# Kernel tuning notes

Hardware: AMD Instinct MI355X
Metric: run time of the kernel (lower is better)

Reference implementation:

```python
import jax, jax.numpy as jnp
import numpy as np

N = 50000        # nodes
E = 800000       # edges (before self-loops)
F_IN = 256       # n_features
HID = 32         # hidden_dims (per-head out channels)
HEADS = 4
HC = HID * HEADS # 128, per-layer width
CLASSES = 40
LAYERS = 2
SLOPE = 0.1      # negative_slope for leaky_relu in attention


def _glorot(key, shape):
    fan_in, fan_out = shape[-2], shape[-1]
    lim = np.sqrt(6.0 / (fan_in + fan_out))
    return jax.random.uniform(key, shape, jnp.float32, -lim, lim)


def setup_inputs() -> dict:
    key = jax.random.key(0)
    ks = jax.random.split(key, 7)
    x = jax.random.normal(ks[0], (N, F_IN), jnp.float32)
    edge_index = jax.random.randint(ks[1], (2, E), 0, N, jnp.int64)
    weight_in = _glorot(ks[2], (F_IN, HC))
    weight_out = _glorot(ks[3], (HC, CLASSES))
    Ws = _glorot(ks[4], (LAYERS, HC, HC))            # per-layer GATConv linear
    atts = _glorot(ks[5], (LAYERS, HEADS, 2 * HID))  # [a_src | a_dst] per head
    biases = jnp.zeros((LAYERS, HC), jnp.float32)
    return {"x": x, "edge_index": edge_index, "weight_in": weight_in,
            "Ws": Ws, "atts": atts, "biases": biases, "weight_out": weight_out}


def _gat_conv(h, src, dst, W, att, bias):
    # h: [N, HC]; src/dst: [E'] edge endpoints (message src -> dst)
    n = h.shape[0]
    hp = (h @ W).reshape(n, HEADS, HID)                       # [N, H, C]
    a_src, a_dst = att[:, :HID], att[:, HID:]                 # [H, C] each
    alpha_src = jnp.einsum('nhc,hc->nh', hp, a_src)           # [N, H]
    alpha_dst = jnp.einsum('nhc,hc->nh', hp, a_dst)
    logits = jax.nn.leaky_relu(alpha_src[src] + alpha_dst[dst], SLOPE)  # [E', H]
    # softmax over edges grouped by destination node
    m = jax.ops.segment_max(logits, dst, num_segments=n)      # [N, H]
    e = jnp.exp(logits - m[dst])
    z = jax.ops.segment_sum(e, dst, num_segments=n)           # [N, H]
    alpha = e / z[dst]                                        # [E', H]
    msg = hp[src] * alpha[:, :, None]                         # [E', H, C]
    out = jax.ops.segment_sum(msg, dst, num_segments=n)       # [N, H, C]
    return out.reshape(n, HC) + bias


def reference(x, edge_index, weight_in, Ws, atts, biases, weight_out):
    # add self-loops (PyG GATConv default)
    loop = jnp.arange(N, dtype=edge_index.dtype)
    src = jnp.concatenate([edge_index[0], loop])
    dst = jnp.concatenate([edge_index[1], loop])
    h = x @ weight_in
    for l in range(LAYERS):
        # dropout is identity in eval mode
        h = jax.nn.elu(_gat_conv(h, src, dst, Ws[l], atts[l], biases[l]))
    return jax.nn.log_softmax(h @ weight_out, axis=1)
```

## Files before the change

kernel.cpp:

```cpp
#include <hip/hip_runtime.h>
#include <hip/hip_bf16.h>
#include <math.h>

#define N_NODES 50000
#define N_EDGES 800000
#define F_IN 256
#define HID 32
#define HEADS 4
#define HC 128
#define CLASSES 40
#define LAYERS 2
#define SLOPE 0.1f
#define EE (N_EDGES + N_NODES)

#define BSHIFT 9
#define NBUCK 98
#define CHUNK 4096
#define NBLK_E ((EE + CHUNK - 1) / CHUNK)
#define GEMM_BLOCKS ((N_NODES + 63) / 64)

typedef unsigned short ushortT;
typedef unsigned int uintT;
typedef __attribute__((ext_vector_type(8))) short short8v;
typedef __attribute__((ext_vector_type(4))) float f32x4;

__device__ __forceinline__ ushortT f2bu(float f) {
    __hip_bfloat16 h = __float2bfloat16(f);
    ushortT u; __builtin_memcpy(&u, &h, 2); return u;
}

__device__ __forceinline__ void scan_buckets(const int* __restrict__ bcnt,
                                             int* sbase, int t) {
    if (t < 64) {
        int i0 = 2 * t, i1 = 2 * t + 1;
        int v0 = (i0 < NBUCK) ? bcnt[i0] : 0;
        int v1 = (i1 < NBUCK) ? bcnt[i1] : 0;
        int s = v0 + v1;
        int x = s;
#pragma unroll
        for (int off = 1; off < 64; off <<= 1) {
            int y = __shfl_up(x, off);
            if (t >= off) x += y;
        }
        int excl = x - s;
        if (i0 <= NBUCK) sbase[i0] = excl;
        if (i1 <= NBUCK) sbase[i1] = excl + v0;
    }
    __syncthreads();
}

__global__ void wconv_all(const float* __restrict__ w_in, const float* __restrict__ Ws,
                          const float* __restrict__ w_out, ushortT* __restrict__ w_inT,
                          ushortT* __restrict__ WsT, ushortT* __restrict__ woutT,
                          int* __restrict__ bcnt, int* __restrict__ gcur0,
                          int* __restrict__ rowptr) {
    int i = blockIdx.x * 256 + threadIdx.x;
    if (i < NBUCK) { bcnt[i] = 0; gcur0[i] = 0; }
    if (i == NBUCK) rowptr[N_NODES] = EE;
    if (i < 32768) {
        int r = i >> 7, c = i & 127;
        w_inT[(size_t)c * F_IN + r] = f2bu(w_in[i]);
    } else if (i < 65536) {
        int j = i - 32768;
        int l = j >> 14, jj = j & 16383;
        int r = jj >> 7, c = jj & 127;
        WsT[l * 16384 + c * 128 + r] = f2bu(Ws[j]);
    } else if (i < 65536 + 6144) {
        int j = i - 65536;
        int c = j >> 7, k = j & 127;
        woutT[j] = (c < CLASSES) ? f2bu(w_out[k * CLASSES + c]) : (ushortT)0;
    }
}

#define AS_LD 40
template<bool AF32>
__device__ __forceinline__ void gemm_body(ushortT* As, ushortT* Bs,
                                          const void* __restrict__ Aptr,
                                          const ushortT* __restrict__ BT,
                                          ushortT* __restrict__ Cb,
                                          const float* __restrict__ att,
                                          float* __restrict__ asrc,
                                          float* __restrict__ adst,
                                          int M, int K, int bid) {
    int t = threadIdx.x;
    int w = t >> 6, lane = t & 63;
    int row0 = bid * 64;
    int ar = t >> 2, ak = (t & 3) * 8;
    int bcol = t >> 1, bks = (t & 1) * 16;
    int wr = w * 16;
    int arow = wr + (lane & 15);
    int ak8 = (lane >> 4) * 8;
    f32x4 acc[8] = {};

    for (int k0 = 0; k0 < K; k0 += 32) {
        int grow = row0 + ar;
        if (AF32) {
            const float* A = (const float*)Aptr;
            float4 v0 = make_float4(0.f, 0.f, 0.f, 0.f), v1 = v0;
            if (grow < M) {
                const float* ap = A + (size_t)grow * K + k0 + ak;
                v0 = *(const float4*)ap;
                v1 = *(const float4*)(ap + 4);
            }
            uint4 p;
            p.x = (uintT)f2bu(v0.x) | ((uintT)f2bu(v0.y) << 16);
            p.y = (uintT)f2bu(v0.z) | ((uintT)f2bu(v0.w) << 16);
            p.z = (uintT)f2bu(v1.x) | ((uintT)f2bu(v1.y) << 16);
            p.w = (uintT)f2bu(v1.z) | ((uintT)f2bu(v1.w) << 16);
            *(uint4*)&As[ar * AS_LD + ak] = p;
        } else {
            const ushortT* A = (const ushortT*)Aptr;
            uint4 p = make_uint4(0, 0, 0, 0);
            if (grow < M) p = *(const uint4*)(A + (size_t)grow * K + k0 + ak);
            *(uint4*)&As[ar * AS_LD + ak] = p;
        }
        {
            const ushortT* bp = BT + (size_t)bcol * K + k0 + bks;
            *(uint4*)&Bs[bcol * AS_LD + bks]     = *(const uint4*)bp;
            *(uint4*)&Bs[bcol * AS_LD + bks + 8] = *(const uint4*)(bp + 8);
        }
        __syncthreads();
        short8v a = *(short8v*)&As[arow * AS_LD + ak8];
#pragma unroll
        for (int c = 0; c < 8; ++c) {
            short8v b = *(short8v*)&Bs[(c * 16 + (lane & 15)) * AS_LD + ak8];
            acc[c] = __builtin_amdgcn_mfma_f32_16x16x32_bf16(a, b, acc[c], 0, 0, 0);
        }
        __syncthreads();
    }
    int cl = lane & 15;
    int r0 = row0 + wr + ((lane >> 4) << 2);
#pragma unroll
    for (int c = 0; c < 8; ++c) {
        int cc = c * 16 + cl;
#pragma unroll
        for (int r = 0; r < 4; ++r) {
            int rr = r0 + r;
            if (rr < M) Cb[(size_t)rr * 128 + cc] = f2bu(acc[c][r]);
        }
    }
    if (att) {
#pragma unroll
        for (int h = 0; h < HEADS; ++h) {
            float as0 = att[h * 64 + cl];
            float as1 = att[h * 64 + 16 + cl];
            float ad0 = att[h * 64 + 32 + cl];
            float ad1 = att[h * 64 + 48 + cl];
#pragma unroll
            for (int r = 0; r < 4; ++r) {
                float ps = acc[2 * h][r] * as0 + acc[2 * h + 1][r] * as1;
                float pd = acc[2 * h][r] * ad0 + acc[2 * h + 1][r] * ad1;
#pragma unroll
                for (int off = 1; off < 16; off <<= 1) {
                    ps += __shfl_xor(ps, off);
                    pd += __shfl_xor(pd, off);
                }
                int rr = r0 + r;
                if (cl == 0 && rr < M) {
                    asrc[rr * 4 + h] = ps;
                    adst[rr * 4 + h] = pd;
                }
            }
        }
    }
}

template<bool AF32>
__global__ __launch_bounds__(256) void gemm_mfma(const void* __restrict__ Aptr,
                                                 const ushortT* __restrict__ BT,
                                                 ushortT* __restrict__ Cb,
                                                 const float* __restrict__ att,
                                                 float* __restrict__ asrc,
                                                 float* __restrict__ adst,
                                                 int M, int K) {
    __shared__ ushortT As[64 * AS_LD];
    __shared__ ushortT Bs[128 * AS_LD];
    gemm_body<AF32>(As, Bs, Aptr, BT, Cb, att, asrc, adst, M, K, blockIdx.x);
}

__device__ __forceinline__ void csr_local_body(const uintT* __restrict__ ebuf,
                                               const int* __restrict__ bcnt,
                                               int* __restrict__ rowptr,
                                               int* __restrict__ ssrc, int b,
                                               int* sbase, int* cnt, int* cur,
                                               int* wsum) {
    int t = threadIdx.x;
    scan_buckets(bcnt, sbase, t);
    int node0 = b << BSHIFT;
    int nb = min(512, N_NODES - node0);
    int beg = sbase[b], end = sbase[b + 1];
    cnt[t] = 0; cnt[t + 256] = 0;
    __syncthreads();
    for (int i = beg + t; i < end; i += 256)
        atomicAdd(&cnt[ebuf[i] & 511], 1);
    __syncthreads();
    int v0 = cnt[2 * t], v1 = cnt[2 * t + 1];
    int s = v0 + v1;
    int lane = t & 63, w = t >> 6;
    int x = s;
#pragma unroll
    for (int off = 1; off < 64; off <<= 1) { int y = __shfl_up(x, off); if (lane >= off) x += y; }
    if (lane == 63) wsum[w] = x;
    __syncthreads();
    if (t == 0) { int run = 0; for (int k = 0; k < 4; ++k) { int tmp = wsum[k]; wsum[k] = run; run += tmp; } }
    __syncthreads();
    int excl = wsum[w] + x - s;
    cnt[2 * t] = excl; cnt[2 * t + 1] = excl + v0;
    cur[2 * t] = excl; cur[2 * t + 1] = excl + v0;
    if (2 * t < nb)     rowptr[node0 + 2 * t]     = beg + excl;
    if (2 * t + 1 < nb) rowptr[node0 + 2 * t + 1] = beg + excl + v0;
    __syncthreads();
    for (int i = beg + t; i < end; i += 256) {
        uintT e = ebuf[i];
        int pos = beg + atomicAdd(&cur[e & 511], 1);
        ssrc[pos] = (int)(e >> BSHIFT);
    }
}

__global__ __launch_bounds__(256) void gemm0_count(const float* __restrict__ x,
                                                   const ushortT* __restrict__ w_inT,
                                                   ushortT* __restrict__ hb0,
                                                   const int* __restrict__ ei,
                                                   int* __restrict__ bcnt) {
    __shared__ ushortT As[64 * AS_LD];
    __shared__ ushortT Bs[128 * AS_LD];
    __shared__ int hist[NBUCK];
    if (blockIdx.x < GEMM_BLOCKS) {
        gemm_body<true>(As, Bs, x, w_inT, hb0, nullptr, nullptr, nullptr,
                        N_NODES, F_IN, blockIdx.x);
    } else {
        int t = threadIdx.x;
        if (t < NBUCK) hist[t] = 0;
        __syncthreads();
        int base = (blockIdx.x - GEMM_BLOCKS) * CHUNK;
        int end = min(base + CHUNK, EE);
        for (int i = base + t; i < end; i += 256) {
            int d = (i < N_EDGES) ? ei[N_EDGES + i] : (i - N_EDGES);
            atomicAdd(&hist[d >> BSHIFT], 1);
        }
        __syncthreads();
        if (t < NBUCK && hist[t]) atomicAdd(&bcnt[t], hist[t]);
    }
}

__global__ __launch_bounds__(256) void gemm_csr(const ushortT* __restrict__ hin,
                                                const ushortT* __restrict__ BT,
                                                ushortT* __restrict__ hpb,
                                                const float* __restrict__ att,
                                                float* __restrict__ asrc,
                                                float* __restrict__ adst,
                                                const uintT* __restrict__ ebuf,
                                                const int* __restrict__ bcnt,
                                                int* __restrict__ rowptr,
                                                int* __restrict__ ssrc) {
    __shared__ ushortT As[64 * AS_LD];
    __shared__ ushortT Bs[128 * AS_LD];
    __shared__ int sbase[NBUCK + 2];
    __shared__ int cnt[512];
    __shared__ int cur[512];
    __shared__ int wsum[4];
    if (blockIdx.x < GEMM_BLOCKS) {
        gemm_body<false>(As, Bs, hin, BT, hpb, att, asrc, adst,
                         N_NODES, HC, blockIdx.x);
    } else {
        csr_local_body(ebuf, bcnt, rowptr, ssrc, blockIdx.x - GEMM_BLOCKS,
                       sbase, cnt, cur, wsum);
    }
}

__global__ __launch_bounds__(256) void bucket_scatter(const int* __restrict__ ei,
                                                      const int* __restrict__ bcnt,
                                                      int* __restrict__ gcur0,
                                                      uintT* __restrict__ ebuf) {
    __shared__ int sbase[NBUCK + 2];
    __shared__ int hist[NBUCK];
    __shared__ int rbase[NBUCK];
    int t = threadIdx.x;
    scan_buckets(bcnt, sbase, t);
    if (t < NBUCK) hist[t] = 0;
    __syncthreads();
    int base = blockIdx.x * CHUNK;
    int end = min(base + CHUNK, EE);
    for (int i = base + t; i < end; i += 256) {
        int d = (i < N_EDGES) ? ei[N_EDGES + i] : (i - N_EDGES);
        atomicAdd(&hist[d >> BSHIFT], 1);
    }
    __syncthreads();
    if (t < NBUCK) {
        int c = hist[t];
        rbase[t] = c ? (sbase[t] + atomicAdd(&gcur0[t], c)) : 0;
    }
    __syncthreads();
    if (t < NBUCK) hist[t] = 0;
    __syncthreads();
    for (int i = base + t; i < end; i += 256) {
        int s, d;
        if (i < N_EDGES) { s = ei[i]; d = ei[N_EDGES + i]; } else { s = d = i - N_EDGES; }
        int b = d >> BSHIFT;
        int pos = rbase[b] + atomicAdd(&hist[b], 1);
        ebuf[pos] = ((uintT)s << BSHIFT) | (uintT)(d & 511);
    }
}

__global__ __launch_bounds__(256) void cls_mfma(const ushortT* __restrict__ A,
                                                const ushortT* __restrict__ BT,
                                                float* __restrict__ out, int M) {
    __shared__ ushortT As[64 * AS_LD];
    __shared__ ushortT Bs[48 * AS_LD];
    int t = threadIdx.x;
    int w = t >> 6, lane = t & 63;
    int row0 = blockIdx.x * 64;
    int ar = t >> 2, ak = (t & 3) * 8;
    int wr = w * 16;
    int arow = wr + (lane & 15);
    int ak8 = (lane >> 4) * 8;
    f32x4 acc[3] = {};

    for (int k0 = 0; k0 < 128; k0 += 32) {
        int grow = row0 + ar;
        uint4 p = make_uint4(0, 0, 0, 0);
        if (grow < M) p = *(const uint4*)(A + (size_t)grow * 128 + k0 + ak);
        *(uint4*)&As[ar * AS_LD + ak] = p;
        if (t < 96) {
            int bcol = t >> 1, bks = (t & 1) * 16;
            const ushortT* bp = BT + bcol * 128 + k0 + bks;
            *(uint4*)&Bs[bcol * AS_LD + bks]     = *(const uint4*)bp;
            *(uint4*)&Bs[bcol * AS_LD + bks + 8] = *(const uint4*)(bp + 8);
        }
        __syncthreads();
        short8v a = *(short8v*)&As[arow * AS_LD + ak8];
#pragma unroll
        for (int c = 0; c < 3; ++c) {
            short8v b = *(short8v*)&Bs[(c * 16 + (lane & 15)) * AS_LD + ak8];
            acc[c] = __builtin_amdgcn_mfma_f32_16x16x32_bf16(a, b, acc[c], 0, 0, 0);
        }
        __syncthreads();
    }
    int cl = lane & 15;
    int r0 = row0 + wr + ((lane >> 4) << 2);
#pragma unroll
    for (int r = 0; r < 4; ++r) {
        float v0 = acc[0][r], v1 = acc[1][r];
        float v2 = (cl < 8) ? acc[2][r] : -1e30f;
        float m = fmaxf(fmaxf(v0, v1), v2);
#pragma unroll
        for (int off = 1; off < 16; off <<= 1) m = fmaxf(m, __shfl_xor(m, off));
        float e = __expf(v0 - m) + __expf(v1 - m) + ((cl < 8) ? __expf(v2 - m) : 0.f);
#pragma unroll
        for (int off = 1; off < 16; off <<= 1) e += __shfl_xor(e, off);
        float ls = m + __logf(e);
        int rr = r0 + r;
        if (rr < M) {
            float* o = out + (size_t)rr * CLASSES;
            o[cl] = v0 - ls;
            o[16 + cl] = v1 - ls;
            if (cl < 8) o[32 + cl] = v2 - ls;
        }
    }
}

__device__ __forceinline__ float lrelu(float v) { return v > 0.f ? v : SLOPE * v; }

__device__ __forceinline__ void gat_one(
    int node, int beg, int deg, int lane,
    const int* __restrict__ ssrc, const float* __restrict__ asrc,
    const float* __restrict__ adst, const ushortT* __restrict__ hpb,
    const float* __restrict__ bias, ushortT* __restrict__ foutB,
    float* sexp, int* ssrcl, float* sm)
{
    float4 ad = *(const float4*)(adst + (size_t)node * 4);
    int g = lane >> 4, i0 = lane & 15;
    float acc0 = 0.f, acc1 = 0.f;
    float zinv;
    const ushortT* hrow = hpb + lane * 2;

    if (deg <= 64) {
        float4 lg = make_float4(-1e30f, -1e30f, -1e30f, -1e30f);
        int soff = 0;
        if (lane < deg) {
            int s = ssrc[beg + lane];
            float4 a = *(const float4*)(asrc + (size_t)s * 4);
            lg.x = lrelu(a.x + ad.x);
            lg.y = lrelu(a.y + ad.y);
            lg.z = lrelu(a.z + ad.z);
            lg.w = lrelu(a.w + ad.w);
            soff = s * HC;
        }
        ssrcl[lane] = soff;
        *(float4*)&sexp[lane * 4] = lg;
        asm volatile("s_waitcnt lgkmcnt(0)" ::: "memory");
        float mg =     sexp[i0 * 4 + g];
        mg = fmaxf(mg, sexp[(i0 + 16) * 4 + g]);
        mg = fmaxf(mg, sexp[(i0 + 32) * 4 + g]);
        mg = fmaxf(mg, sexp[(i0 + 48) * 4 + g]);
#pragma unroll
        for (int off = 1; off < 16; off <<= 1) mg = fmaxf(mg, __shfl_xor(mg, off));
        if (i0 == 0) sm[g] = mg;
        asm volatile("s_waitcnt lgkmcnt(0)" ::: "memory");
        float4 m = *(float4*)&sm[0];
        float4 ex;
        ex.x = __expf(lg.x - m.x);
        ex.y = __expf(lg.y - m.y);
        ex.z = __expf(lg.z - m.z);
        ex.w = __expf(lg.w - m.w);
        *(float4*)&sexp[lane * 4] = ex;
        asm volatile("s_waitcnt lgkmcnt(0)" ::: "memory");
        float zg = sexp[i0 * 4 + g];
        zg +=      sexp[(i0 + 16) * 4 + g];
        zg +=      sexp[(i0 + 32) * 4 + g];
        zg +=      sexp[(i0 + 48) * 4 + g];
#pragma unroll
        for (int off = 1; off < 16; off <<= 1) zg += __shfl_xor(zg, off);
        zinv = 1.f / zg;
#pragma unroll 4
        for (int i = 0; i < deg; ++i) {
            float e = sexp[i * 4 + g];
            int off = ssrcl[i];
            uintT u = *(const uintT*)(hrow + off);
            acc0 = fmaf(__uint_as_float(u << 16),         e, acc0);
            acc1 = fmaf(__uint_as_float(u & 0xffff0000u), e, acc1);
        }
    } else {
        float4 m = make_float4(-1e30f, -1e30f, -1e30f, -1e30f);
        for (int i = lane; i < deg; i += 64) {
            int s = ssrc[beg + i];
            float4 a = *(const float4*)(asrc + (size_t)s * 4);
            m.x = fmaxf(m.x, lrelu(a.x + ad.x));
            m.y = fmaxf(m.y, lrelu(a.y + ad.y));
            m.z = fmaxf(m.z, lrelu(a.z + ad.z));
            m.w = fmaxf(m.w, lrelu(a.w + ad.w));
        }
#pragma unroll
        for (int off = 1; off < 64; off <<= 1) {
            m.x = fmaxf(m.x, __shfl_xor(m.x, off));
            m.y = fmaxf(m.y, __shfl_xor(m.y, off));
            m.z = fmaxf(m.z, __shfl_xor(m.z, off));
            m.w = fmaxf(m.w, __shfl_xor(m.w, off));
        }
        float4 zp = make_float4(0.f, 0.f, 0.f, 0.f);
        for (int c0 = 0; c0 < deg; c0 += 64) {
            int n_ch = min(64, deg - c0);
            if (lane < n_ch) {
                int s = ssrc[beg + c0 + lane];
                float4 a = *(const float4*)(asrc + (size_t)s * 4);
                float4 ex;
                ex.x = __expf(lrelu(a.x + ad.x) - m.x);
                ex.y = __expf(lrelu(a.y + ad.y) - m.y);
                ex.z = __expf(lrelu(a.z + ad.z) - m.z);
                ex.w = __expf(lrelu(a.w + ad.w) - m.w);
                *(float4*)&sexp[lane * 4] = ex;
                ssrcl[lane] = s * HC;
                zp.x += ex.x; zp.y += ex.y; zp.z += ex.z; zp.w += ex.w;
            }
            asm volatile("s_waitcnt lgkmcnt(0)" ::: "memory");
#pragma unroll 4
            for (int i = 0; i < n_ch; ++i) {
                float e = sexp[i * 4 + g];
                int off = ssrcl[i];
                uintT u = *(const uintT*)(hrow + off);
                acc0 = fmaf(__uint_as_float(u << 16),         e, acc0);
                acc1 = fmaf(__uint_as_float(u & 0xffff0000u), e, acc1);
            }
        }
#pragma unroll
        for (int off = 1; off < 64; off <<= 1) {
            zp.x += __shfl_xor(zp.x, off);
            zp.y += __shfl_xor(zp.y, off);
            zp.z += __shfl_xor(zp.z, off);
            zp.w += __shfl_xor(zp.w, off);
        }
        float zh = (g == 0) ? zp.x : (g == 1) ? zp.y : (g == 2) ? zp.z : zp.w;
        zinv = 1.f / zh;
    }

    float b0 = bias[lane * 2], b1 = bias[lane * 2 + 1];
    float v0 = acc0 * zinv + b0; v0 = v0 > 0.f ? v0 : __expf(v0) - 1.f;
    float v1 = acc1 * zinv + b1; v1 = v1 > 0.f ? v1 : __expf(v1) - 1.f;
    *(uintT*)(foutB + (size_t)node * HC + lane * 2) =
        (uintT)f2bu(v0) | ((uintT)f2bu(v1) << 16);
}

#define WPB 4
__global__ __launch_bounds__(256) void gat_gather2(
    const int* __restrict__ rowptr, const int* __restrict__ ssrc,
    const float* __restrict__ asrc, const float* __restrict__ adst,
    const ushortT* __restrict__ hpb, const float* __restrict__ bias,
    ushortT* __restrict__ foutB)
{
    __shared__ __align__(16) float s_exp[WPB][64][4];
    __shared__ int   s_src[WPB][64];
    __shared__ __align__(16) float s_m[WPB][8];
    __shared__ __align__(16) float s_z[WPB][8];
    int w = threadIdx.x >> 6;
    int lane = threadIdx.x & 63;
    int widx = blockIdx.x * WPB + w;
    int n0 = widx * 2;
    if (n0 >= N_NODES) return;
    int beg0 = rowptr[n0];
    int mid  = rowptr[n0 + 1];
    int end1 = rowptr[n0 + 2];
    int deg0 = mid - beg0, deg1 = end1 - mid;

    if (deg0 <= 32 && deg1 <= 32) {
        int half = lane >> 5;
        int ll = lane & 31;
        int nn = n0 + half;
        int mybeg = half ? mid : beg0;
        int mydeg = half ? deg1 : deg0;
        float4 ad = *(const float4*)(adst + (size_t)nn * 4);
        float4 lg = make_float4(-1e30f, -1e30f, -1e30f, -1e30f);
        int soff = 0;
        if (ll < mydeg) {
            int s = ssrc[mybeg + ll];
            float4 a = *(const float4*)(asrc + (size_t)s * 4);
            lg.x = lrelu(a.x + ad.x);
            lg.y = lrelu(a.y + ad.y);
            lg.z = lrelu(a.z + ad.z);
            lg.w = lrelu(a.w + ad.w);
            soff = s * HC;
        }
        s_src[w][lane] = soff;
        *(float4*)&s_exp[w][lane][0] = lg;
        asm volatile("s_waitcnt lgkmcnt(0)" ::: "memory");
        int grp = lane >> 3, gi = lane & 7;
        int gbase = (grp >> 2) << 5;
        int gh = grp & 3;
        float mg =     s_exp[w][gbase + gi][gh];
        mg = fmaxf(mg, s_exp[w][gbase + gi +  8][gh]);
        mg = fmaxf(mg, s_exp[w][gbase + gi + 16][gh]);
        mg = fmaxf(mg, s_exp[w][gbase + gi + 24][gh]);
        mg = fmaxf(mg, __shfl_xor(mg, 1));
        mg = fmaxf(mg, __shfl_xor(mg, 2));
        mg = fmaxf(mg, __shfl_xor(mg, 4));
        if (gi == 0) s_m[w][grp] = mg;
        asm volatile("s_waitcnt lgkmcnt(0)" ::: "memory");
        float4 m = *(float4*)&s_m[w][half * 4];
        float4 ex;
        ex.x = __expf(lg.x - m.x);
        ex.y = __expf(lg.y - m.y);
        ex.z = __expf(lg.z - m.z);
        ex.w = __expf(lg.w - m.w);
        *(float4*)&s_exp[w][lane][0] = ex;
        asm volatile("s_waitcnt lgkmcnt(0)" ::: "memory");
        float zg = s_exp[w][gbase + gi][gh];
        zg +=      s_exp[w][gbase + gi +  8][gh];
        zg +=      s_exp[w][gbase + gi + 16][gh];
        zg +=      s_exp[w][gbase + gi + 24][gh];
        zg += __shfl_xor(zg, 1);
        zg += __shfl_xor(zg, 2);
        zg += __shfl_xor(zg, 4);
        if (gi == 0) s_z[w][grp] = zg;
        asm volatile("s_waitcnt lgkmcnt(0)" ::: "memory");
        int hd = ll >> 3;
        float zinv = 1.f / s_z[w][half * 4 + hd];
        int maxdeg = max(deg0, deg1);
        int ebase = half << 5;
        const ushortT* hrow = hpb + ll * 4;
        float a0 = 0.f, a1 = 0.f, a2 = 0.f, a3 = 0.f;
#pragma unroll 4
        for (int i = 0; i < maxdeg; ++i) {
            float e = s_exp[w][ebase + i][hd];
            int off = s_src[w][ebase + i];
            uint2 u = *(const uint2*)(hrow + off);
            a0 = fmaf(__uint_as_float(u.x << 16),         e, a0);
            a1 = fmaf(__uint_as_float(u.x & 0xffff0000u), e, a1);
            a2 = fmaf(__uint_as_float(u.y << 16),         e, a2);
            a3 = fmaf(__uint_as_float(u.y & 0xffff0000u), e, a3);
        }
        const float* bp = bias + ll * 4;
        float v0 = a0 * zinv + bp[0]; v0 = v0 > 0.f ? v0 : __expf(v0) - 1.f;
        float v1 = a1 * zinv + bp[1]; v1 = v1 > 0.f ? v1 : __expf(v1) - 1.f;
        float v2 = a2 * zinv + bp[2]; v2 = v2 > 0.f ? v2 : __expf(v2) - 1.f;
        float v3 = a3 * zinv + bp[3]; v3 = v3 > 0.f ? v3 : __expf(v3) - 1.f;
        uint2 o;
        o.x = (uintT)f2bu(v0) | ((uintT)f2bu(v1) << 16);
        o.y = (uintT)f2bu(v2) | ((uintT)f2bu(v3) << 16);
        *(uint2*)(foutB + (size_t)nn * HC + ll * 4) = o;
    } else {
        gat_one(n0,     beg0, deg0, lane, ssrc, asrc, adst, hpb, bias, foutB,
                &s_exp[w][0][0], &s_src[w][0], &s_m[w][0]);
        gat_one(n0 + 1, mid,  deg1, lane, ssrc, asrc, adst, hpb, bias, foutB,
                &s_exp[w][0][0], &s_src[w][0], &s_m[w][0]);
    }
}

extern "C" void kernel_launch(void* const* d_in, const int* in_sizes, int n_in,
                              void* d_out, int out_size, void* d_ws, size_t ws_size,
                              hipStream_t stream) {
    const float* x      = (const float*)d_in[0];
    const int*   ei     = (const int*)d_in[1];
    const float* w_in   = (const float*)d_in[2];
    const float* Ws     = (const float*)d_in[3];
    const float* atts   = (const float*)d_in[4];
    const float* biases = (const float*)d_in[5];
    const float* w_out  = (const float*)d_in[6];
    float* out = (float*)d_out;

    char* wp = (char*)d_ws;
    ushortT* hb0 = (ushortT*)wp; wp += (size_t)N_NODES * HC * 2;
    ushortT* hb1 = (ushortT*)wp; wp += (size_t)N_NODES * HC * 2;
    ushortT* hpb = (ushortT*)wp; wp += (size_t)N_NODES * HC * 2;
    float* asrc  = (float*)wp;   wp += (size_t)N_NODES * HEADS * 4;
    float* adst  = (float*)wp;   wp += (size_t)N_NODES * HEADS * 4;
    int* rowptr  = (int*)wp;     wp += (size_t)(N_NODES + 4) * 4;
    int* ssrc    = (int*)wp;     wp += (size_t)EE * 4;
    uintT* ebuf  = (uintT*)wp;   wp += (size_t)EE * 4;
    int* bcnt    = (int*)wp;     wp += (size_t)(NBUCK + 4) * 4;
    int* gcur0   = (int*)wp;     wp += (size_t)(NBUCK + 4) * 4;
    ushortT* w_inT = (ushortT*)wp; wp += (size_t)HC * F_IN * 2;
    ushortT* WsT   = (ushortT*)wp; wp += (size_t)LAYERS * HC * HC * 2;
    ushortT* woutT = (ushortT*)wp; wp += (size_t)48 * HC * 2;

    wconv_all<<<(32768 + 32768 + 6144 + 255) / 256, 256, 0, stream>>>(
        w_in, Ws, w_out, w_inT, WsT, woutT, bcnt, gcur0, rowptr);

    gemm0_count<<<GEMM_BLOCKS + NBLK_E, 256, 0, stream>>>(x, w_inT, hb0, ei, bcnt);

    bucket_scatter<<<NBLK_E, 256, 0, stream>>>(ei, bcnt, gcur0, ebuf);

    gemm_csr<<<GEMM_BLOCKS + NBUCK, 256, 0, stream>>>(
        hb0, WsT, hpb, atts, asrc, adst, ebuf, bcnt, rowptr, ssrc);

    int g2blk = (N_NODES / 2 + WPB - 1) / WPB;
    gat_gather2<<<g2blk, 64 * WPB, 0, stream>>>(
        rowptr, ssrc, asrc, adst, hpb, biases, hb1);

    gemm_mfma<false><<<GEMM_BLOCKS, 256, 0, stream>>>(
        hb1, WsT + (size_t)HC * HC, hpb, atts + (size_t)HEADS * 2 * HID,
        asrc, adst, N_NODES, HC);
    gat_gather2<<<g2blk, 64 * WPB, 0, stream>>>(
        rowptr, ssrc, asrc, adst, hpb, biases + HC, hb0);

    cls_mfma<<<GEMM_BLOCKS, 256, 0, stream>>>(hb0, woutT, out, N_NODES);
}
```

Before: 165.9 us.

## Fuse edge bucketing into one pass using fixed-capacity buckets

```diff
diff --git a/kernel.cpp b/kernel.cpp
--- a/kernel.cpp
+++ b/kernel.cpp
@@ -15,6 +15,7 @@
 
 #define BSHIFT 9
 #define NBUCK 98
+#define BCAP 16384
 #define CHUNK 4096
 #define NBLK_E ((EE + CHUNK - 1) / CHUNK)
 #define GEMM_BLOCKS ((N_NODES + 63) / 64)
@@ -29,34 +30,12 @@
     ushortT u; __builtin_memcpy(&u, &h, 2); return u;
 }
 
-__device__ __forceinline__ void scan_buckets(const int* __restrict__ bcnt,
-                                             int* sbase, int t) {
-    if (t < 64) {
-        int i0 = 2 * t, i1 = 2 * t + 1;
-        int v0 = (i0 < NBUCK) ? bcnt[i0] : 0;
-        int v1 = (i1 < NBUCK) ? bcnt[i1] : 0;
-        int s = v0 + v1;
-        int x = s;
-#pragma unroll
-        for (int off = 1; off < 64; off <<= 1) {
-            int y = __shfl_up(x, off);
-            if (t >= off) x += y;
-        }
-        int excl = x - s;
-        if (i0 <= NBUCK) sbase[i0] = excl;
-        if (i1 <= NBUCK) sbase[i1] = excl + v0;
-    }
-    __syncthreads();
-}
-
 __global__ void wconv_all(const float* __restrict__ w_in, const float* __restrict__ Ws,
                           const float* __restrict__ w_out, ushortT* __restrict__ w_inT,
                           ushortT* __restrict__ WsT, ushortT* __restrict__ woutT,
-                          int* __restrict__ bcnt, int* __restrict__ gcur0,
-                          int* __restrict__ rowptr) {
+                          int* __restrict__ gcur) {
     int i = blockIdx.x * 256 + threadIdx.x;
-    if (i < NBUCK) { bcnt[i] = 0; gcur0[i] = 0; }
-    if (i == NBUCK) rowptr[N_NODES] = EE;
+    if (i < NBUCK) gcur[i] = 0;
     if (i < 32768) {
         int r = i >> 7, c = i & 127;
         w_inT[(size_t)c * F_IN + r] = f2bu(w_in[i]);
@@ -178,17 +157,57 @@
     gemm_body<AF32>(As, Bs, Aptr, BT, Cb, att, asrc, adst, M, K, blockIdx.x);
 }
 
+__global__ __launch_bounds__(256) void gemm0_scatter(const float* __restrict__ x,
+                                                     const ushortT* __restrict__ w_inT,
+                                                     ushortT* __restrict__ hb0,
+                                                     const int* __restrict__ ei,
+                                                     int* __restrict__ gcur,
+                                                     uintT* __restrict__ ebuf) {
+    __shared__ ushortT As[64 * AS_LD];
+    __shared__ ushortT Bs[128 * AS_LD];
+    __shared__ int hist[NBUCK];
+    __shared__ int rbase[NBUCK];
+    if (blockIdx.x < GEMM_BLOCKS) {
+        gemm_body<true>(As, Bs, x, w_inT, hb0, nullptr, nullptr, nullptr,
+                        N_NODES, F_IN, blockIdx.x);
+    } else {
+        int t = threadIdx.x;
+        if (t < NBUCK) hist[t] = 0;
+        __syncthreads();
+        int base = (blockIdx.x - GEMM_BLOCKS) * CHUNK;
+        int end = min(base + CHUNK, EE);
+        for (int i = base + t; i < end; i += 256) {
+            int d = (i < N_EDGES) ? ei[N_EDGES + i] : (i - N_EDGES);
+            atomicAdd(&hist[d >> BSHIFT], 1);
+        }
+        __syncthreads();
+        if (t < NBUCK) {
+            int c = hist[t];
+            rbase[t] = c ? (t * BCAP + atomicAdd(&gcur[t], c)) : 0;
+        }
+        __syncthreads();
+        if (t < NBUCK) hist[t] = 0;
+        __syncthreads();
+        for (int i = base + t; i < end; i += 256) {
+            int s, d;
+            if (i < N_EDGES) { s = ei[i]; d = ei[N_EDGES + i]; } else { s = d = i - N_EDGES; }
+            int b = d >> BSHIFT;
+            int pos = rbase[b] + atomicAdd(&hist[b], 1);
+            ebuf[pos] = ((uintT)s << BSHIFT) | (uintT)(d & 511);
+        }
+    }
+}
+
 __device__ __forceinline__ void csr_local_body(const uintT* __restrict__ ebuf,
-                                               const int* __restrict__ bcnt,
-                                               int* __restrict__ rowptr,
+                                               const int* __restrict__ gcur,
+                                               int2* __restrict__ rowinfo,
                                                int* __restrict__ ssrc, int b,
-                                               int* sbase, int* cnt, int* cur,
-                                               int* wsum) {
+                                               int* cnt, int* cur, int* wsum) {
     int t = threadIdx.x;
-    scan_buckets(bcnt, sbase, t);
     int node0 = b << BSHIFT;
     int nb = min(512, N_NODES - node0);
-    int beg = sbase[b], end = sbase[b + 1];
+    int beg = b * BCAP;
+    int end = beg + gcur[b];
     cnt[t] = 0; cnt[t + 256] = 0;
     __syncthreads();
     for (int i = beg + t; i < end; i += 256)
@@ -207,39 +226,13 @@
     int excl = wsum[w] + x - s;
     cnt[2 * t] = excl; cnt[2 * t + 1] = excl + v0;
     cur[2 * t] = excl; cur[2 * t + 1] = excl + v0;
-    if (2 * t < nb)     rowptr[node0 + 2 * t]     = beg + excl;
-    if (2 * t + 1 < nb) rowptr[node0 + 2 * t + 1] = beg + excl + v0;
+    if (2 * t < nb)     rowinfo[node0 + 2 * t]     = make_int2(beg + excl, v0);
+    if (2 * t + 1 < nb) rowinfo[node0 + 2 * t + 1] = make_int2(beg + excl + v0, v1);
     __syncthreads();
     for (int i = beg + t; i < end; i += 256) {
         uintT e = ebuf[i];
         int pos = beg + atomicAdd(&cur[e & 511], 1);
         ssrc[pos] = (int)(e >> BSHIFT);
-    }
-}
-
-__global__ __launch_bounds__(256) void gemm0_count(const float* __restrict__ x,
-                                                   const ushortT* __restrict__ w_inT,
-                                                   ushortT* __restrict__ hb0,
-                                                   const int* __restrict__ ei,
-                                                   int* __restrict__ bcnt) {
-    __shared__ ushortT As[64 * AS_LD];
-    __shared__ ushortT Bs[128 * AS_LD];
-    __shared__ int hist[NBUCK];
-    if (blockIdx.x < GEMM_BLOCKS) {
-        gemm_body<true>(As, Bs, x, w_inT, hb0, nullptr, nullptr, nullptr,
-                        N_NODES, F_IN, blockIdx.x);
-    } else {
-        int t = threadIdx.x;
-        if (t < NBUCK) hist[t] = 0;
-        __syncthreads();
-        int base = (blockIdx.x - GEMM_BLOCKS) * CHUNK;
-        int end = min(base + CHUNK, EE);
-        for (int i = base + t; i < end; i += 256) {
-            int d = (i < N_EDGES) ? ei[N_EDGES + i] : (i - N_EDGES);
-            atomicAdd(&hist[d >> BSHIFT], 1);
-        }
-        __syncthreads();
-        if (t < NBUCK && hist[t]) atomicAdd(&bcnt[t], hist[t]);
     }
 }
 
@@ -250,12 +243,11 @@
                                                 float* __restrict__ asrc,
                                                 float* __restrict__ adst,
                                                 const uintT* __restrict__ ebuf,
-                                                const int* __restrict__ bcnt,
-                                                int* __restrict__ rowptr,
+                                                const int* __restrict__ gcur,
+                                                int2* __restrict__ rowinfo,
                                                 int* __restrict__ ssrc) {
     __shared__ ushortT As[64 * AS_LD];
     __shared__ ushortT Bs[128 * AS_LD];
-    __shared__ int sbase[NBUCK + 2];
     __shared__ int cnt[512];
     __shared__ int cur[512];
     __shared__ int wsum[4];
@@ -263,42 +255,8 @@
         gemm_body<false>(As, Bs, hin, BT, hpb, att, asrc, adst,
                          N_NODES, HC, blockIdx.x);
     } else {
-        csr_local_body(ebuf, bcnt, rowptr, ssrc, blockIdx.x - GEMM_BLOCKS,
-                       sbase, cnt, cur, wsum);
-    }
-}
-
-__global__ __launch_bounds__(256) void bucket_scatter(const int* __restrict__ ei,
-                                                      const int* __restrict__ bcnt,
-                                                      int* __restrict__ gcur0,
-                                                      uintT* __restrict__ ebuf) {
-    __shared__ int sbase[NBUCK + 2];
-    __shared__ int hist[NBUCK];
-    __shared__ int rbase[NBUCK];
-    int t = threadIdx.x;
-    scan_buckets(bcnt, sbase, t);
-    if (t < NBUCK) hist[t] = 0;
-    __syncthreads();
-    int base = blockIdx.x * CHUNK;
-    int end = min(base + CHUNK, EE);
-    for (int i = base + t; i < end; i += 256) {
-        int d = (i < N_EDGES) ? ei[N_EDGES + i] : (i - N_EDGES);
-        atomicAdd(&hist[d >> BSHIFT], 1);
-    }
-    __syncthreads();
-    if (t < NBUCK) {
-        int c = hist[t];
-        rbase[t] = c ? (sbase[t] + atomicAdd(&gcur0[t], c)) : 0;
-    }
-    __syncthreads();
-    if (t < NBUCK) hist[t] = 0;
-    __syncthreads();
-    for (int i = base + t; i < end; i += 256) {
-        int s, d;
-        if (i < N_EDGES) { s = ei[i]; d = ei[N_EDGES + i]; } else { s = d = i - N_EDGES; }
-        int b = d >> BSHIFT;
-        int pos = rbase[b] + atomicAdd(&hist[b], 1);
-        ebuf[pos] = ((uintT)s << BSHIFT) | (uintT)(d & 511);
+        csr_local_body(ebuf, gcur, rowinfo, ssrc, blockIdx.x - GEMM_BLOCKS,
+                       cnt, cur, wsum);
     }
 }
 
@@ -482,7 +440,7 @@
 
 #define WPB 4
 __global__ __launch_bounds__(256) void gat_gather2(
-    const int* __restrict__ rowptr, const int* __restrict__ ssrc,
+    const int2* __restrict__ rowinfo, const int* __restrict__ ssrc,
     const float* __restrict__ asrc, const float* __restrict__ adst,
     const ushortT* __restrict__ hpb, const float* __restrict__ bias,
     ushortT* __restrict__ foutB)
@@ -496,16 +454,16 @@
     int widx = blockIdx.x * WPB + w;
     int n0 = widx * 2;
     if (n0 >= N_NODES) return;
-    int beg0 = rowptr[n0];
-    int mid  = rowptr[n0 + 1];
-    int end1 = rowptr[n0 + 2];
-    int deg0 = mid - beg0, deg1 = end1 - mid;
+    int2 ri0 = rowinfo[n0];
+    int2 ri1 = rowinfo[n0 + 1];
+    int beg0 = ri0.x, deg0 = ri0.y;
+    int beg1 = ri1.x, deg1 = ri1.y;
 
     if (deg0 <= 32 && deg1 <= 32) {
         int half = lane >> 5;
         int ll = lane & 31;
         int nn = n0 + half;
-        int mybeg = half ? mid : beg0;
+        int mybeg = half ? beg1 : beg0;
         int mydeg = half ? deg1 : deg0;
         float4 ad = *(const float4*)(adst + (size_t)nn * 4);
         float4 lg = make_float4(-1e30f, -1e30f, -1e30f, -1e30f);
@@ -579,7 +537,7 @@
     } else {
         gat_one(n0,     beg0, deg0, lane, ssrc, asrc, adst, hpb, bias, foutB,
                 &s_exp[w][0][0], &s_src[w][0], &s_m[w][0]);
-        gat_one(n0 + 1, mid,  deg1, lane, ssrc, asrc, adst, hpb, bias, foutB,
+        gat_one(n0 + 1, beg1, deg1, lane, ssrc, asrc, adst, hpb, bias, foutB,
                 &s_exp[w][0][0], &s_src[w][0], &s_m[w][0]);
     }
 }
@@ -602,34 +560,31 @@
     ushortT* hpb = (ushortT*)wp; wp += (size_t)N_NODES * HC * 2;
     float* asrc  = (float*)wp;   wp += (size_t)N_NODES * HEADS * 4;
     float* adst  = (float*)wp;   wp += (size_t)N_NODES * HEADS * 4;
-    int* rowptr  = (int*)wp;     wp += (size_t)(N_NODES + 4) * 4;
-    int* ssrc    = (int*)wp;     wp += (size_t)EE * 4;
-    uintT* ebuf  = (uintT*)wp;   wp += (size_t)EE * 4;
-    int* bcnt    = (int*)wp;     wp += (size_t)(NBUCK + 4) * 4;
-    int* gcur0   = (int*)wp;     wp += (size_t)(NBUCK + 4) * 4;
+    int2* rowinfo = (int2*)wp;   wp += (size_t)N_NODES * 8;
+    int* ssrc    = (int*)wp;     wp += (size_t)NBUCK * BCAP * 4;
+    uintT* ebuf  = (uintT*)wp;   wp += (size_t)NBUCK * BCAP * 4;
+    int* gcur    = (int*)wp;     wp += (size_t)(NBUCK + 4) * 4;
     ushortT* w_inT = (ushortT*)wp; wp += (size_t)HC * F_IN * 2;
     ushortT* WsT   = (ushortT*)wp; wp += (size_t)LAYERS * HC * HC * 2;
     ushortT* woutT = (ushortT*)wp; wp += (size_t)48 * HC * 2;
 
     wconv_all<<<(32768 + 32768 + 6144 + 255) / 256, 256, 0, stream>>>(
-        w_in, Ws, w_out, w_inT, WsT, woutT, bcnt, gcur0, rowptr);
-
-    gemm0_count<<<GEMM_BLOCKS + NBLK_E, 256, 0, stream>>>(x, w_inT, hb0, ei, bcnt);
-
-    bucket_scatter<<<NBLK_E, 256, 0, stream>>>(ei, bcnt, gcur0, ebuf);
+        w_in, Ws, w_out, w_inT, WsT, woutT, gcur);
+
+    gemm0_scatter<<<GEMM_BLOCKS + NBLK_E, 256, 0, stream>>>(x, w_inT, hb0, ei, gcur, ebuf);
 
     gemm_csr<<<GEMM_BLOCKS + NBUCK, 256, 0, stream>>>(
-        hb0, WsT, hpb, atts, asrc, adst, ebuf, bcnt, rowptr, ssrc);
+        hb0, WsT, hpb, atts, asrc, adst, ebuf, gcur, rowinfo, ssrc);
 
     int g2blk = (N_NODES / 2 + WPB - 1) / WPB;
     gat_gather2<<<g2blk, 64 * WPB, 0, stream>>>(
-        rowptr, ssrc, asrc, adst, hpb, biases, hb1);
+        rowinfo, ssrc, asrc, adst, hpb, biases, hb1);
 
     gemm_mfma<false><<<GEMM_BLOCKS, 256, 0, stream>>>(
         hb1, WsT + (size_t)HC * HC, hpb, atts + (size_t)HEADS * 2 * HID,
         asrc, adst, N_NODES, HC);
     gat_gather2<<<g2blk, 64 * WPB, 0, stream>>>(
-        rowptr, ssrc, asrc, adst, hpb, biases + HC, hb0);
+        rowinfo, ssrc, asrc, adst, hpb, biases + HC, hb0);
 
     cls_mfma<<<GEMM_BLOCKS, 256, 0, stream>>>(hb0, woutT, out, N_NODES);
 }
```

Measured after the change: 152.0 us, median of 2. -8.3%, faster.
